# Kernel optimization log

Hardware: AMD Instinct MI355X
Metric: run time of the kernel (lower is better)

Reference implementation:

```python
import jax, jax.numpy as jnp
import numpy as np

B, C, H, W = 16, 64, 128, 128
HX, HY = 64, 64


def _rnn_scan(x, Wih, Whh, bih, bhh):
    """Vanilla tanh RNN, batch_first. x: [N, T, Cin] -> [N, T, Hh]."""
    # precompute input projection with one big GEMM
    pre = jnp.einsum('ntc,hc->nth', x, Wih) + bih + bhh  # [N,T,Hh]
    N = x.shape[0]
    h0 = jnp.zeros((N, Whh.shape[0]), dtype=x.dtype)

    def step(h, p):
        h = jnp.tanh(p + h @ Whh.T)
        return h, h

    _, ys = jax.lax.scan(step, h0, jnp.swapaxes(pre, 0, 1))  # [T,N,Hh]
    return jnp.swapaxes(ys, 0, 1)


def setup_inputs() -> dict:
    key = jax.random.key(0)
    ks = jax.random.split(key, 9)
    sx = 1.0 / np.sqrt(HX)
    sy = 1.0 / np.sqrt(HY)
    return {
        'x': jax.random.normal(ks[0], (B, C, H, W), dtype=jnp.float32),
        'Wih_x': jax.random.uniform(ks[1], (HX, C), jnp.float32, -sx, sx),
        'Whh_x': jax.random.uniform(ks[2], (HX, HX), jnp.float32, -sx, sx),
        'bih_x': jax.random.uniform(ks[3], (HX,), jnp.float32, -sx, sx),
        'bhh_x': jax.random.uniform(ks[4], (HX,), jnp.float32, -sx, sx),
        'Wih_y': jax.random.uniform(ks[5], (HY, HX), jnp.float32, -sy, sy),
        'Whh_y': jax.random.uniform(ks[6], (HY, HY), jnp.float32, -sy, sy),
        'bih_y': jax.random.uniform(ks[7], (HY,), jnp.float32, -sy, sy),
        'bhh_y': jax.random.uniform(ks[8], (HY,), jnp.float32, -sy, sy),
    }


def reference(x, Wih_x, Whh_x, bih_x, bhh_x, Wih_y, Whh_y, bih_y, bhh_y):
    b, c, h, w = x.shape
    # X-axis RNN: scan along width, sequences are rows
    xw = jnp.transpose(x, (0, 2, 3, 1)).reshape(b * h, w, c)  # [B*H, W, C]
    out_x = _rnn_scan(xw, Wih_x, Whh_x, bih_x, bhh_x)          # [B*H, W, HX]
    # Y-axis RNN: scan along height, sequences are columns
    xy = out_x.reshape(b, h, w, HX)
    xy = jnp.transpose(xy, (0, 2, 1, 3)).reshape(b * w, h, HX)  # [B*W, H, HX]
    out_y = _rnn_scan(xy, Wih_y, Whh_y, bih_y, bhh_y)           # [B*W, H, HY]
    out = out_y.reshape(b, w, h, HY)
    return jnp.transpose(out, (0, 3, 2, 1))  # [B, HY, H, W]
```

## Files before the change

### kernel.cpp

```cpp
#include <hip/hip_runtime.h>
#include <stdint.h>


#define TLEN 128

typedef __bf16 bf16x8 __attribute__((ext_vector_type(8)));
typedef float  f32x4  __attribute__((ext_vector_type(4)));
typedef unsigned short u16x4 __attribute__((ext_vector_type(4)));

static __device__ __forceinline__ float bf2f(unsigned short s){
    union { unsigned int u; float f; } v; v.u = ((unsigned int)s) << 16; return v.f;
}
static __device__ __forceinline__ unsigned short f2bf(float f){
    union { float f; unsigned int u; } v; v.f = f;
    return (unsigned short)((v.u + 0x7FFFu + ((v.u >> 16) & 1u)) >> 16);
}
static __device__ __forceinline__ __bf16 us2b(unsigned short s){
    union { unsigned short u; __bf16 b; } v; v.u = s; return v.b;
}
struct bfpair { __bf16 hi, lo; };
static __device__ __forceinline__ bfpair splitf(float f){
    unsigned short h = f2bf(f);
    bfpair r;
    r.hi = us2b(h);
    r.lo = us2b(f2bf(f - bf2f(h)));
    return r;
}
static __device__ __forceinline__ float fast_tanh(float x){
    float e = __builtin_amdgcn_exp2f(x * 2.8853900817779268f);
    return 1.0f - 2.0f * __builtin_amdgcn_rcpf(e + 1.0f);
}

template<int PASS>
__global__ __launch_bounds__(256) void k_proj(const float* __restrict__ A,
                                              const float* __restrict__ Wih,
                                              const float* __restrict__ b1,
                                              const float* __restrict__ b2,
                                              float* __restrict__ pre){
    int lane = threadIdx.x & 63;
    int wv   = threadIdx.x >> 6;
    int q    = lane >> 4, l15 = lane & 15;

    bf16x8 Whi[4][2], Wlo[4][2];
#pragma unroll
    for (int n = 0; n < 4; n++)
#pragma unroll
        for (int kc = 0; kc < 2; kc++){
            const float* p = Wih + (n * 16 + l15) * 64 + kc * 32 + q * 8;
#pragma unroll
            for (int i = 0; i < 8; i++){
                bfpair s = splitf(p[i]);
                Whi[n][kc][i] = s.hi;
                Wlo[n][kc][i] = s.lo;
            }
        }
    float bias[4];
#pragma unroll
    for (int n = 0; n < 4; n++){
        int j = n * 16 + l15;
        bias[n] = b1[j] + b2[j];
    }

    int row0 = blockIdx.x * 128 + wv * 32;
#pragma unroll
    for (int mi = 0; mi < 2; mi++){
        int rb = row0 + mi * 16;
        int r  = rb + l15;
        float av[2][8];
        if constexpr (PASS == 0){
            int b = r >> 14, hw = r & 16383;
            const float* xb = A + (size_t)b * 1048576 + hw;
#pragma unroll
            for (int kc = 0; kc < 2; kc++)
#pragma unroll
                for (int i = 0; i < 8; i++)
                    av[kc][i] = xb[(size_t)(kc * 32 + q * 8 + i) * 16384];
        } else {
            int b = r >> 14, w = (r >> 7) & 127, h = r & 127;
            const float* xb = A + ((size_t)((b * 128 + h) * 128 + w)) * 64;
#pragma unroll
            for (int kc = 0; kc < 2; kc++){
                f32x4 v0 = *(const f32x4*)(xb + kc * 32 + q * 8);
                f32x4 v1 = *(const f32x4*)(xb + kc * 32 + q * 8 + 4);
#pragma unroll
                for (int i = 0; i < 4; i++){ av[kc][i] = v0[i]; av[kc][4 + i] = v1[i]; }
            }
        }
        bf16x8 Ahi[2], Alo[2];
#pragma unroll
        for (int kc = 0; kc < 2; kc++)
#pragma unroll
            for (int i = 0; i < 8; i++){
                bfpair s = splitf(av[kc][i]);
                Ahi[kc][i] = s.hi;
                Alo[kc][i] = s.lo;
            }

        f32x4 acc[4];
#pragma unroll
        for (int n = 0; n < 4; n++) acc[n] = (f32x4){bias[n], bias[n], bias[n], bias[n]};
#pragma unroll
        for (int n = 0; n < 4; n++)
#pragma unroll
            for (int kc = 0; kc < 2; kc++){
                acc[n] = __builtin_amdgcn_mfma_f32_16x16x32_bf16(Ahi[kc], Whi[n][kc], acc[n], 0, 0, 0);
                acc[n] = __builtin_amdgcn_mfma_f32_16x16x32_bf16(Alo[kc], Whi[n][kc], acc[n], 0, 0, 0);
                acc[n] = __builtin_amdgcn_mfma_f32_16x16x32_bf16(Ahi[kc], Wlo[n][kc], acc[n], 0, 0, 0);
            }
#pragma unroll
        for (int n = 0; n < 4; n++)
#pragma unroll
            for (int rr = 0; rr < 4; rr++)
                pre[(size_t)(rb + q * 4 + rr) * 64 + n * 16 + l15] = acc[n][rr];
    }
}

template<int PASS>
__global__ __launch_bounds__(256) void k_scan(const float* __restrict__ pre,
                                              const float* __restrict__ Whh,
                                              float* __restrict__ out){
    __shared__ alignas(16) unsigned short hbuf[2][16][2][72];
    int lane = threadIdx.x & 63;
    int wv   = threadIdx.x >> 6;
    int q = lane >> 4, l15 = lane & 15;
    int n0 = blockIdx.x * 16;

    bf16x8 Ahi[2], Alo[2];
#pragma unroll
    for (int kc = 0; kc < 2; kc++){
        const float* p = Whh + (wv * 16 + l15) * 64 + kc * 32 + q * 8;
#pragma unroll
        for (int i = 0; i < 8; i++){
            bfpair s = splitf(p[i]);
            Ahi[kc][i] = s.hi;
            Alo[kc][i] = s.lo;
        }
    }
    bf16x8 Bhi[2], Blo[2];
#pragma unroll
    for (int kc = 0; kc < 2; kc++)
#pragma unroll
        for (int i = 0; i < 8; i++){ Bhi[kc][i] = us2b(0); Blo[kc][i] = us2b(0); }

    int bb = n0 >> 7, w0 = n0 & 127;

    const float* prow = pre + (size_t)(n0 + l15) * TLEN * 64 + wv * 16 + q * 4;
    f32x4 cur = *(const f32x4*)prow;

    for (int t = 0; t < TLEN; t++){
        f32x4 nxt = (f32x4){0.f, 0.f, 0.f, 0.f};
        if (t < TLEN - 1) nxt = *(const f32x4*)(prow + (size_t)(t + 1) * 64);

        f32x4 acc = cur;
#pragma unroll
        for (int kc = 0; kc < 2; kc++){
            acc = __builtin_amdgcn_mfma_f32_16x16x32_bf16(Ahi[kc], Bhi[kc], acc, 0, 0, 0);
            acc = __builtin_amdgcn_mfma_f32_16x16x32_bf16(Ahi[kc], Blo[kc], acc, 0, 0, 0);
            acc = __builtin_amdgcn_mfma_f32_16x16x32_bf16(Alo[kc], Bhi[kc], acc, 0, 0, 0);
        }
        int par = t & 1;
        int j0  = wv * 16 + q * 4;
        float tv[4];
        u16x4 hi4, lo4;
#pragma unroll
        for (int r = 0; r < 4; r++){
            tv[r] = fast_tanh(acc[r]);
            unsigned short h = f2bf(tv[r]);
            hi4[r] = h;
            lo4[r] = f2bf(tv[r] - bf2f(h));
        }
        *(u16x4*)&hbuf[par][l15][0][j0] = hi4;
        *(u16x4*)&hbuf[par][l15][1][j0] = lo4;

        if constexpr (PASS == 0){
            f32x4 ov = (f32x4){tv[0], tv[1], tv[2], tv[3]};
            *(f32x4*)(out + ((size_t)(n0 + l15) * TLEN + t) * 64 + j0) = ov;
        } else {
#pragma unroll
            for (int r = 0; r < 4; r++)
                out[((size_t)(bb * 64 + j0 + r) * TLEN + t) * 128 + w0 + l15] = tv[r];
        }
        __syncthreads();
#pragma unroll
        for (int kc = 0; kc < 2; kc++){
            Bhi[kc] = *(const bf16x8*)&hbuf[par][l15][0][kc * 32 + q * 8];
            Blo[kc] = *(const bf16x8*)&hbuf[par][l15][1][kc * 32 + q * 8];
        }
        cur = nxt;
    }
}

extern "C" void kernel_launch(void* const* d_in, const int* in_sizes, int n_in,
                              void* d_out, int out_size, void* d_ws, size_t ws_size,
                              hipStream_t stream){
    (void)in_sizes; (void)n_in; (void)out_size; (void)ws_size;
    const float* x    = (const float*)d_in[0];
    const float* Wihx = (const float*)d_in[1];
    const float* Whhx = (const float*)d_in[2];
    const float* bihx = (const float*)d_in[3];
    const float* bhhx = (const float*)d_in[4];
    const float* Wihy = (const float*)d_in[5];
    const float* Whhy = (const float*)d_in[6];
    const float* bihy = (const float*)d_in[7];
    const float* bhhy = (const float*)d_in[8];
    float* ob  = (float*)d_out;
    float* pre = (float*)d_ws;

    k_proj<0><<<2048, 256, 0, stream>>>(x,  Wihx, bihx, bhhx, pre);
    k_scan<0><<<128,  256, 0, stream>>>(pre, Whhx, ob);
    k_proj<1><<<2048, 256, 0, stream>>>(ob, Wihy, bihy, bhhy, pre);
    k_scan<1><<<128,  256, 0, stream>>>(pre, Whhy, ob);
}
```

Baseline: 261.7 us.

## Store intermediate in fp16, time-major pre layout, split MFMA chains, swizzled LDS

The X-pass hidden output is now stored as fp16 and read back as fp16 MFMA operands in the Y projection, which needs 2 instead of 3 MFMAs per tile. The projection buffer is written time-major so each scan step reads a contiguous slab, prefetched 4 steps ahead. In the scan, the three dependent MFMAs per chunk are split into independent accumulators to shorten the dependency chain. It also adds an XOR-swizzled unpadded LDS layout, a lighter barrier and hoisted projection loads. The fp16 intermediate and single-split products reduce precision for the Y pass.

```diff
diff --git a/kernel.cpp b/kernel.cpp
--- a/kernel.cpp
+++ b/kernel.cpp
@@ -3,9 +3,12 @@
 
 
 #define TLEN 128
-
-typedef __bf16 bf16x8 __attribute__((ext_vector_type(8)));
-typedef float  f32x4  __attribute__((ext_vector_type(4)));
+#define NSEQ 2048
+#define PSTRIDE (NSEQ * 64)
+
+typedef __bf16   bf16x8 __attribute__((ext_vector_type(8)));
+typedef _Float16 f16x8  __attribute__((ext_vector_type(8)));
+typedef float    f32x4  __attribute__((ext_vector_type(4)));
 typedef unsigned short u16x4 __attribute__((ext_vector_type(4)));
 
 static __device__ __forceinline__ float bf2f(unsigned short s){
@@ -21,18 +24,23 @@
 struct bfpair { __bf16 hi, lo; };
 static __device__ __forceinline__ bfpair splitf(float f){
     unsigned short h = f2bf(f);
-    bfpair r;
-    r.hi = us2b(h);
-    r.lo = us2b(f2bf(f - bf2f(h)));
-    return r;
+    bfpair r; r.hi = us2b(h); r.lo = us2b(f2bf(f - bf2f(h))); return r;
+}
+struct hpair { _Float16 hi, lo; };
+static __device__ __forceinline__ hpair splith(float f){
+    hpair r; r.hi = (_Float16)f; r.lo = (_Float16)(f - (float)r.hi); return r;
 }
 static __device__ __forceinline__ float fast_tanh(float x){
     float e = __builtin_amdgcn_exp2f(x * 2.8853900817779268f);
     return 1.0f - 2.0f * __builtin_amdgcn_rcpf(e + 1.0f);
 }
+static __device__ __forceinline__ void lds_barrier(){
+    asm volatile("s_waitcnt lgkmcnt(0)\n\ts_barrier" ::: "memory");
+}
 
 template<int PASS>
-__global__ __launch_bounds__(256) void k_proj(const float* __restrict__ A,
+__global__ __launch_bounds__(256) void k_proj(const float* __restrict__ A32,
+                                              const unsigned short* __restrict__ A16,
                                               const float* __restrict__ Wih,
                                               const float* __restrict__ b1,
                                               const float* __restrict__ b2,
@@ -41,7 +49,8 @@
     int wv   = threadIdx.x >> 6;
     int q    = lane >> 4, l15 = lane & 15;
 
-    bf16x8 Whi[4][2], Wlo[4][2];
+    bf16x8 Wbh[4][2], Wbl[4][2];
+    f16x8  Wfh[4][2], Wfl[4][2];
 #pragma unroll
     for (int n = 0; n < 4; n++)
 #pragma unroll
@@ -49,9 +58,13 @@
             const float* p = Wih + (n * 16 + l15) * 64 + kc * 32 + q * 8;
 #pragma unroll
             for (int i = 0; i < 8; i++){
-                bfpair s = splitf(p[i]);
-                Whi[n][kc][i] = s.hi;
-                Wlo[n][kc][i] = s.lo;
+                if constexpr (PASS == 0){
+                    bfpair s = splitf(p[i]);
+                    Wbh[n][kc][i] = s.hi; Wbl[n][kc][i] = s.lo;
+                } else {
+                    hpair s = splith(p[i]);
+                    Wfh[n][kc][i] = s.hi; Wfl[n][kc][i] = s.lo;
+                }
             }
         }
     float bias[4];
@@ -62,64 +75,78 @@
     }
 
     int row0 = blockIdx.x * 128 + wv * 32;
+
+    float av[2][2][8];
+    f16x8 Af[2][2];
+#pragma unroll
+    for (int mi = 0; mi < 2; mi++){
+        int r = row0 + mi * 16 + l15;
+        if constexpr (PASS == 0){
+            int b = r >> 14, hw = r & 16383;
+            const float* xb = A32 + (size_t)b * 1048576 + hw;
+#pragma unroll
+            for (int kc = 0; kc < 2; kc++)
+#pragma unroll
+                for (int i = 0; i < 8; i++)
+                    av[mi][kc][i] = xb[(size_t)(kc * 32 + q * 8 + i) * 16384];
+        } else {
+            int b = r >> 14, w = (r >> 7) & 127, h = r & 127;
+            const unsigned short* xb = A16 + ((size_t)((b * 128 + h) * 128 + w)) * 64;
+#pragma unroll
+            for (int kc = 0; kc < 2; kc++)
+                Af[mi][kc] = *(const f16x8*)(xb + kc * 32 + q * 8);
+        }
+    }
+
 #pragma unroll
     for (int mi = 0; mi < 2; mi++){
         int rb = row0 + mi * 16;
-        int r  = rb + l15;
-        float av[2][8];
+        f32x4 acc[4];
+#pragma unroll
+        for (int n = 0; n < 4; n++) acc[n] = (f32x4){bias[n], bias[n], bias[n], bias[n]};
+
         if constexpr (PASS == 0){
-            int b = r >> 14, hw = r & 16383;
-            const float* xb = A + (size_t)b * 1048576 + hw;
+            bf16x8 Ahi[2], Alo[2];
 #pragma unroll
             for (int kc = 0; kc < 2; kc++)
 #pragma unroll
-                for (int i = 0; i < 8; i++)
-                    av[kc][i] = xb[(size_t)(kc * 32 + q * 8 + i) * 16384];
+                for (int i = 0; i < 8; i++){
+                    bfpair s = splitf(av[mi][kc][i]);
+                    Ahi[kc][i] = s.hi; Alo[kc][i] = s.lo;
+                }
+#pragma unroll
+            for (int n = 0; n < 4; n++)
+#pragma unroll
+                for (int kc = 0; kc < 2; kc++){
+                    acc[n] = __builtin_amdgcn_mfma_f32_16x16x32_bf16(Ahi[kc], Wbh[n][kc], acc[n], 0, 0, 0);
+                    acc[n] = __builtin_amdgcn_mfma_f32_16x16x32_bf16(Alo[kc], Wbh[n][kc], acc[n], 0, 0, 0);
+                    acc[n] = __builtin_amdgcn_mfma_f32_16x16x32_bf16(Ahi[kc], Wbl[n][kc], acc[n], 0, 0, 0);
+                }
         } else {
-            int b = r >> 14, w = (r >> 7) & 127, h = r & 127;
-            const float* xb = A + ((size_t)((b * 128 + h) * 128 + w)) * 64;
-#pragma unroll
-            for (int kc = 0; kc < 2; kc++){
-                f32x4 v0 = *(const f32x4*)(xb + kc * 32 + q * 8);
-                f32x4 v1 = *(const f32x4*)(xb + kc * 32 + q * 8 + 4);
-#pragma unroll
-                for (int i = 0; i < 4; i++){ av[kc][i] = v0[i]; av[kc][4 + i] = v1[i]; }
-            }
-        }
-        bf16x8 Ahi[2], Alo[2];
-#pragma unroll
-        for (int kc = 0; kc < 2; kc++)
-#pragma unroll
-            for (int i = 0; i < 8; i++){
-                bfpair s = splitf(av[kc][i]);
-                Ahi[kc][i] = s.hi;
-                Alo[kc][i] = s.lo;
-            }
-
-        f32x4 acc[4];
-#pragma unroll
-        for (int n = 0; n < 4; n++) acc[n] = (f32x4){bias[n], bias[n], bias[n], bias[n]};
+#pragma unroll
+            for (int n = 0; n < 4; n++)
+#pragma unroll
+                for (int kc = 0; kc < 2; kc++){
+                    acc[n] = __builtin_amdgcn_mfma_f32_16x16x32_f16(Af[mi][kc], Wfh[n][kc], acc[n], 0, 0, 0);
+                    acc[n] = __builtin_amdgcn_mfma_f32_16x16x32_f16(Af[mi][kc], Wfl[n][kc], acc[n], 0, 0, 0);
+                }
+        }
+        int lo7 = rb & 127;
+        int baseSM = (rb >> 14) * 128 + ((rb >> 7) & 127);
 #pragma unroll
         for (int n = 0; n < 4; n++)
 #pragma unroll
-            for (int kc = 0; kc < 2; kc++){
-                acc[n] = __builtin_amdgcn_mfma_f32_16x16x32_bf16(Ahi[kc], Whi[n][kc], acc[n], 0, 0, 0);
-                acc[n] = __builtin_amdgcn_mfma_f32_16x16x32_bf16(Alo[kc], Whi[n][kc], acc[n], 0, 0, 0);
-                acc[n] = __builtin_amdgcn_mfma_f32_16x16x32_bf16(Ahi[kc], Wlo[n][kc], acc[n], 0, 0, 0);
-            }
-#pragma unroll
-        for (int n = 0; n < 4; n++)
-#pragma unroll
             for (int rr = 0; rr < 4; rr++)
-                pre[(size_t)(rb + q * 4 + rr) * 64 + n * 16 + l15] = acc[n][rr];
+                pre[(size_t)((lo7 + q * 4 + rr) * 2048 + baseSM) * 64 + n * 16 + l15] = acc[n][rr];
     }
 }
 
 template<int PASS>
 __global__ __launch_bounds__(256) void k_scan(const float* __restrict__ pre,
                                               const float* __restrict__ Whh,
-                                              float* __restrict__ out){
-    __shared__ alignas(16) unsigned short hbuf[2][16][2][72];
+                                              unsigned short* __restrict__ outh,
+                                              float* __restrict__ outf){
+    __shared__ alignas(16) unsigned short hbuf[2][2][16][64];
     int lane = threadIdx.x & 63;
     int wv   = threadIdx.x >> 6;
     int q = lane >> 4, l15 = lane & 15;
@@ -132,8 +159,7 @@
 #pragma unroll
         for (int i = 0; i < 8; i++){
             bfpair s = splitf(p[i]);
-            Ahi[kc][i] = s.hi;
-            Alo[kc][i] = s.lo;
+            Ahi[kc][i] = s.hi; Alo[kc][i] = s.lo;
         }
     }
     bf16x8 Bhi[2], Blo[2];
@@ -144,49 +170,68 @@
 
     int bb = n0 >> 7, w0 = n0 & 127;
 
-    const float* prow = pre + (size_t)(n0 + l15) * TLEN * 64 + wv * 16 + q * 4;
-    f32x4 cur = *(const f32x4*)prow;
-
-    for (int t = 0; t < TLEN; t++){
-        f32x4 nxt = (f32x4){0.f, 0.f, 0.f, 0.f};
-        if (t < TLEN - 1) nxt = *(const f32x4*)(prow + (size_t)(t + 1) * 64);
-
-        f32x4 acc = cur;
-#pragma unroll
-        for (int kc = 0; kc < 2; kc++){
-            acc = __builtin_amdgcn_mfma_f32_16x16x32_bf16(Ahi[kc], Bhi[kc], acc, 0, 0, 0);
-            acc = __builtin_amdgcn_mfma_f32_16x16x32_bf16(Ahi[kc], Blo[kc], acc, 0, 0, 0);
-            acc = __builtin_amdgcn_mfma_f32_16x16x32_bf16(Alo[kc], Bhi[kc], acc, 0, 0, 0);
-        }
-        int par = t & 1;
-        int j0  = wv * 16 + q * 4;
-        float tv[4];
-        u16x4 hi4, lo4;
-#pragma unroll
-        for (int r = 0; r < 4; r++){
-            tv[r] = fast_tanh(acc[r]);
-            unsigned short h = f2bf(tv[r]);
-            hi4[r] = h;
-            lo4[r] = f2bf(tv[r] - bf2f(h));
-        }
-        *(u16x4*)&hbuf[par][l15][0][j0] = hi4;
-        *(u16x4*)&hbuf[par][l15][1][j0] = lo4;
-
-        if constexpr (PASS == 0){
-            f32x4 ov = (f32x4){tv[0], tv[1], tv[2], tv[3]};
-            *(f32x4*)(out + ((size_t)(n0 + l15) * TLEN + t) * 64 + j0) = ov;
-        } else {
-#pragma unroll
-            for (int r = 0; r < 4; r++)
-                out[((size_t)(bb * 64 + j0 + r) * TLEN + t) * 128 + w0 + l15] = tv[r];
-        }
-        __syncthreads();
-#pragma unroll
-        for (int kc = 0; kc < 2; kc++){
-            Bhi[kc] = *(const bf16x8*)&hbuf[par][l15][0][kc * 32 + q * 8];
-            Blo[kc] = *(const bf16x8*)&hbuf[par][l15][1][kc * 32 + q * 8];
-        }
-        cur = nxt;
+    const float* pb = pre + (size_t)(n0 + l15) * 64 + wv * 16 + q * 4;
+    f32x4 buf[4];
+#pragma unroll
+    for (int d = 0; d < 4; d++) buf[d] = *(const f32x4*)(pb + (size_t)d * PSTRIDE);
+
+    int j0 = wv * 16 + q * 4;
+    int e  = l15 & 7;
+    int wj  = (((j0 >> 3) ^ e) << 3) | (j0 & 7);
+    int rj0 = ((q)     ^ e) << 3;
+    int rj1 = ((4 + q) ^ e) << 3;
+
+    for (int t = 0; t < TLEN; t += 4){
+#pragma unroll
+        for (int u = 0; u < 4; u++){
+            int tt = t + u;
+            f32x4 cur = buf[u];
+            int tn = tt + 4;
+            if (tn < TLEN) buf[u] = *(const f32x4*)(pb + (size_t)tn * PSTRIDE);
+
+            f32x4 a0 = cur;
+            f32x4 a1 = (f32x4){0.f, 0.f, 0.f, 0.f};
+            f32x4 a2 = (f32x4){0.f, 0.f, 0.f, 0.f};
+            a0 = __builtin_amdgcn_mfma_f32_16x16x32_bf16(Ahi[0], Bhi[0], a0, 0, 0, 0);
+            a1 = __builtin_amdgcn_mfma_f32_16x16x32_bf16(Ahi[0], Blo[0], a1, 0, 0, 0);
+            a2 = __builtin_amdgcn_mfma_f32_16x16x32_bf16(Alo[0], Bhi[0], a2, 0, 0, 0);
+            a0 = __builtin_amdgcn_mfma_f32_16x16x32_bf16(Ahi[1], Bhi[1], a0, 0, 0, 0);
+            a1 = __builtin_amdgcn_mfma_f32_16x16x32_bf16(Ahi[1], Blo[1], a1, 0, 0, 0);
+            a2 = __builtin_amdgcn_mfma_f32_16x16x32_bf16(Alo[1], Bhi[1], a2, 0, 0, 0);
+            f32x4 acc = (a0 + a1) + a2;
+
+            float tv[4]; u16x4 hi4, lo4;
+#pragma unroll
+            for (int r = 0; r < 4; r++){
+                tv[r] = fast_tanh(acc[r]);
+                unsigned short h = f2bf(tv[r]);
+                hi4[r] = h;
+                lo4[r] = f2bf(tv[r] - bf2f(h));
+            }
+            int par = tt & 1;
+            *(u16x4*)&hbuf[par][0][l15][wj] = hi4;
+            *(u16x4*)&hbuf[par][1][l15][wj] = lo4;
+
+            if constexpr (PASS == 0){
+                u16x4 ov;
+#pragma unroll
+                for (int r = 0; r < 4; r++){
+                    union { _Float16 h; unsigned short s; } c;
+                    c.h = (_Float16)tv[r];
+                    ov[r] = c.s;
+                }
+                *(u16x4*)(outh + ((size_t)(n0 + l15) * TLEN + tt) * 64 + j0) = ov;
+            } else {
+#pragma unroll
+                for (int r = 0; r < 4; r++)
+                    outf[((size_t)(bb * 64 + j0 + r) * TLEN + tt) * 128 + w0 + l15] = tv[r];
+            }
+            lds_barrier();
+            Bhi[0] = *(const bf16x8*)&hbuf[par][0][l15][rj0];
+            Blo[0] = *(const bf16x8*)&hbuf[par][1][l15][rj0];
+            Bhi[1] = *(const bf16x8*)&hbuf[par][0][l15][rj1];
+            Blo[1] = *(const bf16x8*)&hbuf[par][1][l15][rj1];
+        }
     }
 }
 
@@ -203,11 +248,12 @@
     const float* Whhy = (const float*)d_in[6];
     const float* bihy = (const float*)d_in[7];
     const float* bhhy = (const float*)d_in[8];
-    float* ob  = (float*)d_out;
     float* pre = (float*)d_ws;
-
-    k_proj<0><<<2048, 256, 0, stream>>>(x,  Wihx, bihx, bhhx, pre);
-    k_scan<0><<<128,  256, 0, stream>>>(pre, Whhx, ob);
-    k_proj<1><<<2048, 256, 0, stream>>>(ob, Wihy, bihy, bhhy, pre);
-    k_scan<1><<<128,  256, 0, stream>>>(pre, Whhy, ob);
-}
+    unsigned short* oxh = (unsigned short*)d_out;
+    float* of = (float*)d_out;
+
+    k_proj<0><<<2048, 256, 0, stream>>>(x, nullptr, Wihx, bihx, bhhx, pre);
+    k_scan<0><<<128,  256, 0, stream>>>(pre, Whhx, oxh, nullptr);
+    k_proj<1><<<2048, 256, 0, stream>>>(nullptr, oxh, Wihy, bihy, bhhy, pre);
+    k_scan<1><<<128,  256, 0, stream>>>(pre, Whhy, nullptr, of);
+}
```

Result: slower. 323.3 us (+23.6%).
